# Kernel tuning notes

Hardware: AMD Instinct MI355X
Metric: run time of the kernel (lower is better)

## Reference

```python
import jax, jax.numpy as jnp
import numpy as np

NUM_RELS = 19


def rgcn_layer(h, W, b, src, dst, etype, n_nodes):
    """DGL RelGraphConv (basis regularizer, num_bases=num_rels, sum aggregation, bias, no self-loop).

    out[v] = sum_{e: dst(e)=v} W[etype(e)] @ h[src(e)] + b
    Computed as: aggregate h[src] per (relation, dst) pair, then one GEMM per relation.
    """
    # segment id combines relation and destination node -> [R*N] segments
    seg = etype * n_nodes + dst
    agg = jax.ops.segment_sum(h[src], seg, num_segments=NUM_RELS * n_nodes)
    agg = agg.reshape(NUM_RELS, n_nodes, h.shape[1])  # [R, N, in]
    return jnp.einsum('rni,rio->no', agg, W) + b       # [N, out]


def setup_inputs() -> dict:
    key = jax.random.key(0)
    ks = jax.random.split(key, 8)
    N, E, R, D = 100000, 1600000, NUM_RELS, 32
    s = 0.1  # keep activations well-scaled across layers
    return {
        'src': jax.random.randint(ks[0], (E,), 0, N, dtype=jnp.int32),
        'dst': jax.random.randint(ks[1], (E,), 0, N, dtype=jnp.int32),
        'etype': jax.random.randint(ks[2], (E,), 0, R, dtype=jnp.int32),
        'n_nodes': N,
        'W1': jax.random.normal(ks[3], (R, 1, D), jnp.float32) * s,
        'b1': jnp.zeros((D,), jnp.float32),
        'W2': jax.random.normal(ks[4], (R, D, D), jnp.float32) * s,
        'b2': jnp.zeros((D,), jnp.float32),
        'W3': jax.random.normal(ks[5], (D, D), jnp.float32) * s,
        'b3': jnp.zeros((D,), jnp.float32),
    }


def reference(src, dst, etype, n_nodes, W1, b1, W2, b2, W3, b3):
    # h = ones(N, 1), as in Embedder.forward
    h = jnp.ones((n_nodes, 1), jnp.float32)
    h = jax.nn.relu(rgcn_layer(h, W1, b1, src, dst, etype, n_nodes))
    h = jax.nn.relu(rgcn_layer(h, W2, b2, src, dst, etype, n_nodes))
    # conv_output=False -> final layer is a plain Linear
    return h @ W3 + b3
```

## Files before the change

### kernel.cpp

```cpp
#include <hip/hip_runtime.h>

#define NUM_RELS 19
#define NPB 256
#define NPB_SHIFT 8
#define MAXB 400
#define NBLK 512

typedef _Float16 half8 __attribute__((ext_vector_type(8)));
typedef float floatx4 __attribute__((ext_vector_type(4)));



__global__ void w2swz_kernel(const float* __restrict__ W2, _Float16* __restrict__ W2F,
                             int* __restrict__ bcnt, int B) {
    int idx = blockIdx.x * blockDim.x + threadIdx.x;
    if (idx < B) bcnt[idx] = 0;
    if (idx >= NUM_RELS * 2 * 64 * 8) return;
    int j = idx & 7, lane = (idx >> 3) & 63, nt = (idx >> 9) & 1, r = idx >> 10;
    int k = (lane >> 4) * 8 + j, n = nt * 16 + (lane & 15);
    W2F[idx] = (_Float16)W2[r * 1024 + k * 32 + n];
}


__global__ __launch_bounds__(512) void count_kernel(const int* __restrict__ dst,
                                                    int* __restrict__ blkhist,
                                                    int* __restrict__ bcnt,
                                                    int E, int B, int chunk) {
    __shared__ int h[MAXB];
    for (int i = threadIdx.x; i < B; i += 512) h[i] = 0;
    __syncthreads();
    int e0 = blockIdx.x * chunk, e1 = min(E, e0 + chunk);
    for (int e = e0 + (int)threadIdx.x; e < e1; e += 512)
        atomicAdd(&h[dst[e] >> NPB_SHIFT], 1);
    __syncthreads();
    for (int i = threadIdx.x; i < B; i += 512) {
        blkhist[blockIdx.x * B + i] = h[i];
        if (h[i]) atomicAdd(&bcnt[i], h[i]);
    }
}


__global__ __launch_bounds__(NBLK) void offscan_kernel(const int* __restrict__ blkhist,
                                                       const int* __restrict__ bcnt,
                                                       int* __restrict__ pbase,
                                                       int* __restrict__ offs, int B) {
    __shared__ int lds[NBLK];
    __shared__ int pbs;
    int bucket = blockIdx.x;
    int t = threadIdx.x;

    int c = (t < B) ? ((bcnt[t] + 7) & ~7) : 0;
    lds[t] = c;
    __syncthreads();
    for (int off = 1; off < NBLK; off <<= 1) {
        int x = (t >= off) ? lds[t - off] : 0;
        __syncthreads();
        lds[t] += x;
        __syncthreads();
    }
    if (t == bucket) {
        pbs = lds[t] - c;
        pbase[bucket] = pbs;
    }
    __syncthreads();
    int myp = pbs;

    int v = blkhist[t * B + bucket];
    lds[t] = v;
    __syncthreads();
    for (int off = 1; off < NBLK; off <<= 1) {
        int x = (t >= off) ? lds[t - off] : 0;
        __syncthreads();
        lds[t] += x;
        __syncthreads();
    }
    offs[t * B + bucket] = myp + lds[t] - v;
}


__global__ __launch_bounds__(512) void scatter2_kernel(
    const int* __restrict__ src, const int* __restrict__ dst, const int* __restrict__ etype,
    const int* __restrict__ offs, unsigned* __restrict__ recs4, int E, int B, int chunk) {
    __shared__ int cur[MAXB];
    for (int i = threadIdx.x; i < B; i += 512) cur[i] = offs[blockIdx.x * B + i];
    __syncthreads();
    int e0 = blockIdx.x * chunk, e1 = min(E, e0 + chunk);
    for (int e = e0 + (int)threadIdx.x; e < e1; e += 512) {
        int d = dst[e];
        int b = d >> NPB_SHIFT;
        int pos = atomicAdd(&cur[b], 1);
        recs4[pos] = ((unsigned)(d & (NPB - 1)) << 22) | ((unsigned)src[e] << 5) | (unsigned)etype[e];
    }
}


__global__ __launch_bounds__(512) void bsort_l1_kernel(
    const unsigned* __restrict__ recs4, const int* __restrict__ pbase, const int* __restrict__ bcnt,
    int* __restrict__ recs2, int* __restrict__ row_start, int* __restrict__ rend,
    const float* __restrict__ W1, const float* __restrict__ b1,
    _Float16* __restrict__ h1, int N) {
    __shared__ int hist[NPB];
    __shared__ int offsl[NPB];
    __shared__ int cnt2[NPB * NUM_RELS];
    __shared__ float W1s[NUM_RELS * 32];
    __shared__ float b1s[32];
    int b = blockIdx.x;
    int p0 = pbase[b], n = bcnt[b];
    int t = threadIdx.x;

    if (t < NPB) hist[t] = 0;
    for (int i = t; i < NPB * NUM_RELS; i += 512) cnt2[i] = 0;
    for (int i = t; i < NUM_RELS * 32; i += 512) W1s[i] = W1[i];
    if (t < 32) b1s[t] = b1[t];
    __syncthreads();

    for (int i = t; i < n; i += 512) {
        unsigned rec = recs4[p0 + i];
        int ln = rec >> 22;
        atomicAdd(&hist[ln], 1);
        atomicAdd(&cnt2[ln * NUM_RELS + (rec & 31)], 1);
    }
    __syncthreads();
    int c = 0;
    if (t < NPB) {
        c = hist[t];
        offsl[t] = c;
    }
    __syncthreads();
    for (int off = 1; off < NPB; off <<= 1) {
        int x = 0;
        if (t < NPB && t >= off) x = offsl[t - off];
        __syncthreads();
        if (t < NPB) offsl[t] += x;
        __syncthreads();
    }
    int v0n = b << NPB_SHIFT;
    if (t < NPB) {
        int start = p0 + offsl[t] - c;
        int v = v0n + t;
        if (v < N) {
            row_start[v] = start;
            rend[v] = start + c;
        }
    }
    __syncthreads();

    int o = t & 31, hw = t >> 5;
    for (int k = hw; k < NPB; k += 16) {
        int vv = v0n + k;
        if (vv < N) {
            float acc = b1s[o];
            const int* cp = &cnt2[k * NUM_RELS];
#pragma unroll
            for (int r = 0; r < NUM_RELS; ++r) acc += (float)cp[r] * W1s[r * 32 + o];
            h1[(size_t)vv * 32 + o] = (_Float16)fmaxf(acc, 0.f);
        }
    }
    __syncthreads();

    if (t < NPB) {
        int base = p0 + offsl[t] - c;
        for (int r = 0; r < NUM_RELS; ++r) {
            int cv = cnt2[t * NUM_RELS + r];
            cnt2[t * NUM_RELS + r] = base;
            base += cv;
        }
    }
    __syncthreads();

    for (int i = t; i < n; i += 512) {
        unsigned rec = recs4[p0 + i];
        int p = atomicAdd(&cnt2[(rec >> 22) * NUM_RELS + (rec & 31)], 1);
        recs2[p] = (int)(rec & 0x3FFFFFu);
    }
}


#define AGG_STRIDE (NUM_RELS * 32 + 4)

__global__ __launch_bounds__(512) void edge23_kernel(
    const _Float16* __restrict__ h1, const int* __restrict__ row_start,
    const int* __restrict__ rend, const int* __restrict__ recs2,
    const _Float16* __restrict__ W2F,
    const float* __restrict__ b2, const float* __restrict__ W3, const float* __restrict__ b3,
    float* __restrict__ out, int N) {
    __shared__ float agg[16 * AGG_STRIDE];
    __shared__ float h2t[16 * 32];
    __shared__ float W3s[1024];
    __shared__ float b2s[32], b3s[32];
    int t = threadIdx.x;
    for (int i = t; i < 16 * AGG_STRIDE; i += 512) agg[i] = 0.f;
    for (int i = t; i < 1024; i += 512) W3s[i] = W3[i];
    if (t < 32) {
        b2s[t] = b2[t];
        b3s[t] = b3[t];
    }
    __syncthreads();

    int o = t & 31;
    int hw = t >> 5;
    int node = blockIdx.x * 16 + hw;
    if (node < N) {
        int start = row_start[node], end = rend[node];
        float* aggn = agg + hw * AGG_STRIDE + o;
        float acc = 0.f;
        int prev_r = -1;
        for (int base = start; base < end; base += 32) {
            int idx = base + o;
            int m_l = (idx < end) ? recs2[idx] : 0;
            int cnt = min(32, end - base);
            int j = 0;
            for (; j + 4 <= cnt; j += 4) {
                int m0 = __shfl(m_l, j, 32);
                int m1 = __shfl(m_l, j + 1, 32);
                int m2 = __shfl(m_l, j + 2, 32);
                int m3 = __shfl(m_l, j + 3, 32);
                float v0 = (float)h1[(size_t)(m0 >> 5) * 32 + o];
                float v1 = (float)h1[(size_t)(m1 >> 5) * 32 + o];
                float v2 = (float)h1[(size_t)(m2 >> 5) * 32 + o];
                float v3 = (float)h1[(size_t)(m3 >> 5) * 32 + o];
                int r0 = m0 & 31, r1 = m1 & 31, r2 = m2 & 31, r3 = m3 & 31;
                acc = (r0 == prev_r) ? (acc + v0) : v0;
                aggn[r0 * 32] = acc;
                acc = (r1 == r0) ? (acc + v1) : v1;
                aggn[r1 * 32] = acc;
                acc = (r2 == r1) ? (acc + v2) : v2;
                aggn[r2 * 32] = acc;
                acc = (r3 == r2) ? (acc + v3) : v3;
                aggn[r3 * 32] = acc;
                prev_r = r3;
            }
            for (; j < cnt; ++j) {
                int m = __shfl(m_l, j, 32);
                int r = m & 31;
                float v = (float)h1[(size_t)(m >> 5) * 32 + o];
                acc = (r == prev_r) ? (acc + v) : v;
                aggn[r * 32] = acc;
                prev_r = r;
            }
        }
    }
    __syncthreads();

    int lane = t & 63;
    int wv = t >> 6;
    if (wv < 2) {
        int nt = wv;
        floatx4 accd = {0.f, 0.f, 0.f, 0.f};
        const float* ap0 = agg + (lane & 15) * AGG_STRIDE + (lane >> 4) * 8;
        for (int r = 0; r < NUM_RELS; ++r) {
            const float* ap = ap0 + r * 32;
            half8 a;
#pragma unroll
            for (int j = 0; j < 8; ++j) a[j] = (_Float16)ap[j];
            half8 bfrag = *(const half8*)(W2F + ((r * 2 + nt) * 64 + lane) * 8);
            accd = __builtin_amdgcn_mfma_f32_16x16x32_f16(a, bfrag, accd, 0, 0, 0);
        }
        int col = lane & 15, rowb = (lane >> 4) * 4;
#pragma unroll
        for (int reg = 0; reg < 4; ++reg) {
            h2t[(rowb + reg) * 32 + nt * 16 + col] = fmaxf(accd[reg] + b2s[nt * 16 + col], 0.f);
        }
    }
    __syncthreads();

    if (node < N) {
        float h2v = h2t[hw * 32 + o];
        float acc3 = b3s[o];
#pragma unroll
        for (int i = 0; i < 32; ++i) {
            float hi = __shfl(h2v, i, 32);
            acc3 = fmaf(hi, W3s[i * 32 + o], acc3);
        }
        out[(size_t)node * 32 + o] = acc3;
    }
}


extern "C" void kernel_launch(void* const* d_in, const int* in_sizes, int n_in,
                              void* d_out, int out_size, void* d_ws, size_t ws_size,
                              hipStream_t stream) {
    const int* src   = (const int*)d_in[0];
    const int* dst   = (const int*)d_in[1];
    const int* etype = (const int*)d_in[2];
    const float* W1  = (const float*)d_in[4];
    const float* b1  = (const float*)d_in[5];
    const float* W2  = (const float*)d_in[6];
    const float* b2  = (const float*)d_in[7];
    const float* W3  = (const float*)d_in[8];
    const float* b3  = (const float*)d_in[9];
    float* out = (float*)d_out;

    int E = in_sizes[0];
    int N = out_size / 32;
    int B = (N + NPB - 1) >> NPB_SHIFT;

    char* ws = (char*)d_ws;
    size_t off = 0;
    auto alloc = [&](size_t bytes) {
        void* p = ws + off;
        off = (off + bytes + 255) & ~(size_t)255;
        return p;
    };
    int* bcnt       = (int*)alloc((size_t)MAXB * 4);
    int* pbase      = (int*)alloc((size_t)MAXB * 4);
    int* blkhist    = (int*)alloc((size_t)NBLK * MAXB * 4);
    int* offs       = (int*)alloc((size_t)NBLK * MAXB * 4);
    int* row_start  = (int*)alloc((size_t)N * 4);
    int* rend       = (int*)alloc((size_t)N * 4);
    unsigned* recs4 = (unsigned*)alloc(((size_t)E + 8 * MAXB + 64) * 4);
    int* recs2      = (int*)alloc(((size_t)E + 8 * MAXB + 64) * 4);
    _Float16* h1    = (_Float16*)alloc(((size_t)N + NPB) * 32 * 2);
    _Float16* W2F   = (_Float16*)alloc((size_t)NUM_RELS * 2 * 64 * 8 * 2);

    w2swz_kernel<<<(NUM_RELS * 2 * 64 * 8 + 255) / 256, 256, 0, stream>>>(W2, W2F, bcnt, B);

    int chunk = (E + NBLK - 1) / NBLK;
    count_kernel<<<NBLK, 512, 0, stream>>>(dst, blkhist, bcnt, E, B, chunk);
    offscan_kernel<<<B, NBLK, 0, stream>>>(blkhist, bcnt, pbase, offs, B);
    scatter2_kernel<<<NBLK, 512, 0, stream>>>(src, dst, etype, offs, recs4, E, B, chunk);

    bsort_l1_kernel<<<B, 512, 0, stream>>>(recs4, pbase, bcnt, recs2, row_start, rend,
                                           W1, b1, h1, N);

    edge23_kernel<<<(N + 15) / 16, 512, 0, stream>>>(h1, row_start, rend, recs2, W2F,
                                                     b2, W3, b3, out, N);
}
```

Baseline: 247.5 us.

## Replace two-level bucket sort with global atomic counting sort on (dst,rel) keys

Replaces the bucketed two-pass sort (per-block histograms, offset scan, bucket scatter, in-block resort) with a direct counting sort. Global atomics build a histogram over dst*19+etype segments, a three-kernel multi-block scan turns it into cursors and row pointers, and a single atomic scatter writes the records. Layer 1 now reads the per-segment counts from the histogram. This drops one full pass over the edge records and the in-LDS resort, but it relies on heavy contended global atomics over 1.9M counters and adds more kernel launches. Scatter order within a segment becomes nondeterministic.

Result: slower. 426.4 us (+72.3%).

```diff
diff --git a/kernel.cpp b/kernel.cpp
--- a/kernel.cpp
+++ b/kernel.cpp
@@ -1,177 +1,132 @@
 #include <hip/hip_runtime.h>
 
 #define NUM_RELS 19
-#define NPB 256
-#define NPB_SHIFT 8
-#define MAXB 400
-#define NBLK 512
 
 typedef _Float16 half8 __attribute__((ext_vector_type(8)));
 typedef float floatx4 __attribute__((ext_vector_type(4)));
 
 
 
-__global__ void w2swz_kernel(const float* __restrict__ W2, _Float16* __restrict__ W2F,
-                             int* __restrict__ bcnt, int B) {
-    int idx = blockIdx.x * blockDim.x + threadIdx.x;
-    if (idx < B) bcnt[idx] = 0;
-    if (idx >= NUM_RELS * 2 * 64 * 8) return;
-    int j = idx & 7, lane = (idx >> 3) & 63, nt = (idx >> 9) & 1, r = idx >> 10;
-    int k = (lane >> 4) * 8 + j, n = nt * 16 + (lane & 15);
-    W2F[idx] = (_Float16)W2[r * 1024 + k * 32 + n];
-}
-
-
-__global__ __launch_bounds__(512) void count_kernel(const int* __restrict__ dst,
-                                                    int* __restrict__ blkhist,
-                                                    int* __restrict__ bcnt,
-                                                    int E, int B, int chunk) {
-    __shared__ int h[MAXB];
-    for (int i = threadIdx.x; i < B; i += 512) h[i] = 0;
-    __syncthreads();
-    int e0 = blockIdx.x * chunk, e1 = min(E, e0 + chunk);
-    for (int e = e0 + (int)threadIdx.x; e < e1; e += 512)
-        atomicAdd(&h[dst[e] >> NPB_SHIFT], 1);
-    __syncthreads();
-    for (int i = threadIdx.x; i < B; i += 512) {
-        blkhist[blockIdx.x * B + i] = h[i];
-        if (h[i]) atomicAdd(&bcnt[i], h[i]);
-    }
-}
-
-
-__global__ __launch_bounds__(NBLK) void offscan_kernel(const int* __restrict__ blkhist,
-                                                       const int* __restrict__ bcnt,
-                                                       int* __restrict__ pbase,
-                                                       int* __restrict__ offs, int B) {
-    __shared__ int lds[NBLK];
-    __shared__ int pbs;
-    int bucket = blockIdx.x;
-    int t = threadIdx.x;
-
-    int c = (t < B) ? ((bcnt[t] + 7) & ~7) : 0;
-    lds[t] = c;
-    __syncthreads();
-    for (int off = 1; off < NBLK; off <<= 1) {
+__global__ __launch_bounds__(512) void w2z_kernel(const float* __restrict__ W2,
+                                                  _Float16* __restrict__ W2F,
+                                                  int* __restrict__ seg, int M) {
+    int idx = blockIdx.x * 512 + threadIdx.x;
+    if (idx < NUM_RELS * 2 * 64 * 8) {
+        int j = idx & 7, lane = (idx >> 3) & 63, nt = (idx >> 9) & 1, r = idx >> 10;
+        int k = (lane >> 4) * 8 + j, n = nt * 16 + (lane & 15);
+        W2F[idx] = (_Float16)W2[r * 1024 + k * 32 + n];
+    }
+    for (int i = idx; i < M; i += gridDim.x * 512) seg[i] = 0;
+}
+
+
+__global__ __launch_bounds__(256) void hist_kernel(const int* __restrict__ dst,
+                                                   const int* __restrict__ etype,
+                                                   int* __restrict__ seg, int E) {
+    int i0 = blockIdx.x * 256 + threadIdx.x;
+    for (int e = i0; e < E; e += gridDim.x * 256)
+        atomicAdd(&seg[dst[e] * NUM_RELS + etype[e]], 1);
+}
+
+
+__global__ __launch_bounds__(512) void scan1_kernel(const int* __restrict__ seg,
+                                                    int* __restrict__ cursor,
+                                                    int* __restrict__ btot, int M) {
+    __shared__ int lds[512];
+    int t = threadIdx.x;
+    int i = blockIdx.x * 512 + t;
+    int v = (i < M) ? seg[i] : 0;
+    lds[t] = v;
+    __syncthreads();
+    for (int off = 1; off < 512; off <<= 1) {
         int x = (t >= off) ? lds[t - off] : 0;
         __syncthreads();
         lds[t] += x;
         __syncthreads();
     }
-    if (t == bucket) {
-        pbs = lds[t] - c;
-        pbase[bucket] = pbs;
-    }
-    __syncthreads();
-    int myp = pbs;
-
-    int v = blkhist[t * B + bucket];
-    lds[t] = v;
-    __syncthreads();
-    for (int off = 1; off < NBLK; off <<= 1) {
-        int x = (t >= off) ? lds[t - off] : 0;
-        __syncthreads();
-        lds[t] += x;
-        __syncthreads();
-    }
-    offs[t * B + bucket] = myp + lds[t] - v;
-}
-
-
-__global__ __launch_bounds__(512) void scatter2_kernel(
-    const int* __restrict__ src, const int* __restrict__ dst, const int* __restrict__ etype,
-    const int* __restrict__ offs, unsigned* __restrict__ recs4, int E, int B, int chunk) {
-    __shared__ int cur[MAXB];
-    for (int i = threadIdx.x; i < B; i += 512) cur[i] = offs[blockIdx.x * B + i];
-    __syncthreads();
-    int e0 = blockIdx.x * chunk, e1 = min(E, e0 + chunk);
-    for (int e = e0 + (int)threadIdx.x; e < e1; e += 512) {
-        int d = dst[e];
-        int b = d >> NPB_SHIFT;
-        int pos = atomicAdd(&cur[b], 1);
-        recs4[pos] = ((unsigned)(d & (NPB - 1)) << 22) | ((unsigned)src[e] << 5) | (unsigned)etype[e];
-    }
-}
-
-
-__global__ __launch_bounds__(512) void bsort_l1_kernel(
-    const unsigned* __restrict__ recs4, const int* __restrict__ pbase, const int* __restrict__ bcnt,
-    int* __restrict__ recs2, int* __restrict__ row_start, int* __restrict__ rend,
-    const float* __restrict__ W1, const float* __restrict__ b1,
-    _Float16* __restrict__ h1, int N) {
-    __shared__ int hist[NPB];
-    __shared__ int offsl[NPB];
-    __shared__ int cnt2[NPB * NUM_RELS];
+    if (i < M) cursor[i] = lds[t] - v;
+    if (t == 511) btot[blockIdx.x] = lds[511];
+}
+
+
+__global__ __launch_bounds__(512) void scan2_kernel(const int* __restrict__ btot,
+                                                    int* __restrict__ bbase, int NB) {
+    __shared__ int lds[512];
+    __shared__ int run;
+    int t = threadIdx.x;
+    if (t == 0) run = 0;
+    __syncthreads();
+    for (int c = 0; c < NB; c += 512) {
+        int i = c + t;
+        int v = (i < NB) ? btot[i] : 0;
+        lds[t] = v;
+        __syncthreads();
+        for (int off = 1; off < 512; off <<= 1) {
+            int x = (t >= off) ? lds[t - off] : 0;
+            __syncthreads();
+            lds[t] += x;
+            __syncthreads();
+        }
+        if (i < NB) bbase[i] = run + lds[t] - v;
+        __syncthreads();
+        if (t == 0) run += lds[511];
+        __syncthreads();
+    }
+}
+
+
+__global__ __launch_bounds__(512) void addback_kernel(int* __restrict__ cursor,
+                                                      const int* __restrict__ bbase,
+                                                      int* __restrict__ rowptr, int M) {
+    int i = blockIdx.x * 512 + threadIdx.x;
+    if (i >= M) return;
+    int val = cursor[i] + bbase[blockIdx.x];
+    cursor[i] = val;
+    unsigned q = (unsigned)i / NUM_RELS;
+    if ((unsigned)i == q * NUM_RELS) rowptr[q] = val;
+}
+
+
+__global__ __launch_bounds__(512) void l1_kernel(const int* __restrict__ seg,
+                                                 const float* __restrict__ W1,
+                                                 const float* __restrict__ b1,
+                                                 _Float16* __restrict__ h1, int N) {
+    __shared__ int cnts[256 * NUM_RELS];
     __shared__ float W1s[NUM_RELS * 32];
     __shared__ float b1s[32];
-    int b = blockIdx.x;
-    int p0 = pbase[b], n = bcnt[b];
-    int t = threadIdx.x;
-
-    if (t < NPB) hist[t] = 0;
-    for (int i = t; i < NPB * NUM_RELS; i += 512) cnt2[i] = 0;
+    int t = threadIdx.x;
+    int v0 = blockIdx.x * 256;
+    int base = v0 * NUM_RELS;
+    int lim = min(256 * NUM_RELS, N * NUM_RELS - base);
+    for (int i = t; i < lim; i += 512) cnts[i] = seg[base + i];
     for (int i = t; i < NUM_RELS * 32; i += 512) W1s[i] = W1[i];
     if (t < 32) b1s[t] = b1[t];
     __syncthreads();
-
-    for (int i = t; i < n; i += 512) {
-        unsigned rec = recs4[p0 + i];
-        int ln = rec >> 22;
-        atomicAdd(&hist[ln], 1);
-        atomicAdd(&cnt2[ln * NUM_RELS + (rec & 31)], 1);
-    }
-    __syncthreads();
-    int c = 0;
-    if (t < NPB) {
-        c = hist[t];
-        offsl[t] = c;
-    }
-    __syncthreads();
-    for (int off = 1; off < NPB; off <<= 1) {
-        int x = 0;
-        if (t < NPB && t >= off) x = offsl[t - off];
-        __syncthreads();
-        if (t < NPB) offsl[t] += x;
-        __syncthreads();
-    }
-    int v0n = b << NPB_SHIFT;
-    if (t < NPB) {
-        int start = p0 + offsl[t] - c;
-        int v = v0n + t;
+    int o = t & 31, hw = t >> 5;
+    for (int k = hw; k < 256; k += 16) {
+        int v = v0 + k;
         if (v < N) {
-            row_start[v] = start;
-            rend[v] = start + c;
-        }
-    }
-    __syncthreads();
-
-    int o = t & 31, hw = t >> 5;
-    for (int k = hw; k < NPB; k += 16) {
-        int vv = v0n + k;
-        if (vv < N) {
             float acc = b1s[o];
-            const int* cp = &cnt2[k * NUM_RELS];
+            const int* cp = &cnts[k * NUM_RELS];
 #pragma unroll
             for (int r = 0; r < NUM_RELS; ++r) acc += (float)cp[r] * W1s[r * 32 + o];
-            h1[(size_t)vv * 32 + o] = (_Float16)fmaxf(acc, 0.f);
-        }
-    }
-    __syncthreads();
-
-    if (t < NPB) {
-        int base = p0 + offsl[t] - c;
-        for (int r = 0; r < NUM_RELS; ++r) {
-            int cv = cnt2[t * NUM_RELS + r];
-            cnt2[t * NUM_RELS + r] = base;
-            base += cv;
-        }
-    }
-    __syncthreads();
-
-    for (int i = t; i < n; i += 512) {
-        unsigned rec = recs4[p0 + i];
-        int p = atomicAdd(&cnt2[(rec >> 22) * NUM_RELS + (rec & 31)], 1);
-        recs2[p] = (int)(rec & 0x3FFFFFu);
+            h1[(size_t)v * 32 + o] = (_Float16)fmaxf(acc, 0.f);
+        }
+    }
+}
+
+
+__global__ __launch_bounds__(256) void scat_kernel(const int* __restrict__ src,
+                                                   const int* __restrict__ dst,
+                                                   const int* __restrict__ etype,
+                                                   int* __restrict__ cursor,
+                                                   int* __restrict__ recs2, int E) {
+    int i0 = blockIdx.x * 256 + threadIdx.x;
+    for (int e = i0; e < E; e += gridDim.x * 256) {
+        int et = etype[e];
+        int key = dst[e] * NUM_RELS + et;
+        int pos = atomicAdd(&cursor[key], 1);
+        recs2[pos] = (src[e] << 5) | et;
     }
 }
 
@@ -293,7 +248,8 @@
 
     int E = in_sizes[0];
     int N = out_size / 32;
-    int B = (N + NPB - 1) >> NPB_SHIFT;
+    int M = N * NUM_RELS + 1;
+    int NB = (M + 511) / 512;
 
     char* ws = (char*)d_ws;
     size_t off = 0;
@@ -302,27 +258,23 @@
         off = (off + bytes + 255) & ~(size_t)255;
         return p;
     };
-    int* bcnt       = (int*)alloc((size_t)MAXB * 4);
-    int* pbase      = (int*)alloc((size_t)MAXB * 4);
-    int* blkhist    = (int*)alloc((size_t)NBLK * MAXB * 4);
-    int* offs       = (int*)alloc((size_t)NBLK * MAXB * 4);
-    int* row_start  = (int*)alloc((size_t)N * 4);
-    int* rend       = (int*)alloc((size_t)N * 4);
-    unsigned* recs4 = (unsigned*)alloc(((size_t)E + 8 * MAXB + 64) * 4);
-    int* recs2      = (int*)alloc(((size_t)E + 8 * MAXB + 64) * 4);
-    _Float16* h1    = (_Float16*)alloc(((size_t)N + NPB) * 32 * 2);
-    _Float16* W2F   = (_Float16*)alloc((size_t)NUM_RELS * 2 * 64 * 8 * 2);
-
-    w2swz_kernel<<<(NUM_RELS * 2 * 64 * 8 + 255) / 256, 256, 0, stream>>>(W2, W2F, bcnt, B);
-
-    int chunk = (E + NBLK - 1) / NBLK;
-    count_kernel<<<NBLK, 512, 0, stream>>>(dst, blkhist, bcnt, E, B, chunk);
-    offscan_kernel<<<B, NBLK, 0, stream>>>(blkhist, bcnt, pbase, offs, B);
-    scatter2_kernel<<<NBLK, 512, 0, stream>>>(src, dst, etype, offs, recs4, E, B, chunk);
-
-    bsort_l1_kernel<<<B, 512, 0, stream>>>(recs4, pbase, bcnt, recs2, row_start, rend,
-                                           W1, b1, h1, N);
-
-    edge23_kernel<<<(N + 15) / 16, 512, 0, stream>>>(h1, row_start, rend, recs2, W2F,
+    int* seg     = (int*)alloc((size_t)M * 4);
+    int* cursor  = (int*)alloc((size_t)M * 4);
+    int* btot    = (int*)alloc((size_t)NB * 4);
+    int* bbase   = (int*)alloc((size_t)NB * 4);
+    int* rowptr  = (int*)alloc(((size_t)N + 2) * 4);
+    int* recs2   = (int*)alloc(((size_t)E + 64) * 4);
+    _Float16* h1 = (_Float16*)alloc(((size_t)N + 256) * 32 * 2);
+    _Float16* W2F = (_Float16*)alloc((size_t)NUM_RELS * 2 * 64 * 8 * 2);
+
+    w2z_kernel<<<512, 512, 0, stream>>>(W2, W2F, seg, M);
+    hist_kernel<<<1024, 256, 0, stream>>>(dst, etype, seg, E);
+    scan1_kernel<<<NB, 512, 0, stream>>>(seg, cursor, btot, M);
+    scan2_kernel<<<1, 512, 0, stream>>>(btot, bbase, NB);
+    addback_kernel<<<NB, 512, 0, stream>>>(cursor, bbase, rowptr, M);
+    l1_kernel<<<(N + 255) / 256, 512, 0, stream>>>(seg, W1, b1, h1, N);
+    scat_kernel<<<1024, 256, 0, stream>>>(src, dst, etype, cursor, recs2, E);
+
+    edge23_kernel<<<(N + 15) / 16, 512, 0, stream>>>(h1, rowptr, rowptr + 1, recs2, W2F,
                                                      b2, W3, b3, out, N);
 }
```
